# Kernel optimization log

Hardware: AMD Instinct MI355X
Metric: run time of the kernel (lower is better)

The kernel has to match this reference:

```python
import jax, jax.numpy as jnp
import numpy as np

N_NODES = 50000
N_EDGES = 800000
IN_DIM = 512
HEADS = 4
HID = 64
OUT = 64
NEG_SLOPE = 0.2  # DGL GATConv default


def gat_layer(x, W, attn_l, attn_r, bias, src, dst, n_nodes, heads, d_out):
    # x: [N, F_in], W: [F_in, heads*d_out], attn_l/attn_r: [heads, d_out], bias: [heads, d_out]
    f = (x @ W).reshape(n_nodes, heads, d_out)          # [N, H, D]
    el = jnp.sum(f * attn_l, axis=-1)                   # [N, H]
    er = jnp.sum(f * attn_r, axis=-1)                   # [N, H]
    e = jax.nn.leaky_relu(el[src] + er[dst], NEG_SLOPE) # [E, H]
    # segment softmax over incoming edges of each dst node
    m = jax.ops.segment_max(e, dst, num_segments=n_nodes)       # [N, H]
    ex = jnp.exp(e - m[dst])                                     # [E, H]
    den = jax.ops.segment_sum(ex, dst, num_segments=n_nodes)    # [N, H]
    a = ex / den[dst]                                            # [E, H]
    # scatter-aggregate weighted messages
    out = jax.ops.segment_sum(a[:, :, None] * f[src], dst, num_segments=n_nodes)  # [N, H, D]
    return out + bias, a


def setup_inputs() -> dict:
    key = jax.random.key(0)
    ks = jax.random.split(key, 12)
    features = jax.random.normal(ks[0], (N_NODES, IN_DIM), dtype=jnp.float32)
    src = jax.random.randint(ks[1], (N_EDGES,), 0, N_NODES, dtype=jnp.int32)
    dst = jax.random.randint(ks[2], (N_EDGES,), 0, N_NODES, dtype=jnp.int32)
    s1 = 1.0 / np.sqrt(IN_DIM)
    s2 = 1.0 / np.sqrt(HEADS * HID)
    W1 = jax.random.normal(ks[3], (IN_DIM, HEADS * HID), dtype=jnp.float32) * s1
    al1 = jax.random.normal(ks[4], (HEADS, HID), dtype=jnp.float32) * s1
    ar1 = jax.random.normal(ks[5], (HEADS, HID), dtype=jnp.float32) * s1
    b1 = jnp.zeros((HEADS, HID), dtype=jnp.float32)
    W2 = jax.random.normal(ks[6], (HEADS * HID, OUT), dtype=jnp.float32) * s2
    al2 = jax.random.normal(ks[7], (1, OUT), dtype=jnp.float32) * s2
    ar2 = jax.random.normal(ks[8], (1, OUT), dtype=jnp.float32) * s2
    b2 = jnp.zeros((1, OUT), dtype=jnp.float32)
    return {"features": features, "W1": W1, "al1": al1, "ar1": ar1, "b1": b1,
            "W2": W2, "al2": al2, "ar2": ar2, "b2": b2, "src": src, "dst": dst}


def reference(features, W1, al1, ar1, b1, W2, al2, ar2, b2, src, dst):
    h1, _ = gat_layer(features, W1, al1, ar1, b1, src, dst, N_NODES, HEADS, HID)
    h1 = jax.nn.elu(h1.reshape(N_NODES, HEADS * HID))   # flatten heads + ELU
    h2, _ = gat_layer(h1, W2, al2, ar2, b2, src, dst, N_NODES, 1, OUT)
    return h2  # [N, 1, OUT]
```

## Files before the change

### kernel.cpp

```cpp
#include <hip/hip_runtime.h>

#define N_NODES 50000
#define N_EDGES 800000
#define IN_DIM 512
#define NEG_SLOPE 0.2f

typedef short short8 __attribute__((ext_vector_type(8)));
typedef float f32x16 __attribute__((ext_vector_type(16)));
typedef __attribute__((address_space(3))) unsigned int lds_u32;
typedef const __attribute__((address_space(1))) unsigned int glb_u32;

__device__ __forceinline__ unsigned bf16rne(float f) {
  union { float f; unsigned u; } v;
  v.f = f;
  return (v.u + 0x7FFFu + ((v.u >> 16) & 1u)) >> 16;
}
__device__ __forceinline__ void tsplit8(float4 a, float4 b, short8& hi,
                                        short8& lo) {
  float fa[8] = {a.x, a.y, a.z, a.w, b.x, b.y, b.z, b.w};
#pragma unroll
  for (int i = 0; i < 8; i++) {
    unsigned u = __float_as_uint(fa[i]);
    hi[i] = (short)(u >> 16);
    float lof = fa[i] - __uint_as_float(u & 0xffff0000u);
    lo[i] = (short)(__float_as_uint(lof) >> 16);
  }
}

__global__ void pack_w(const float* __restrict__ W, short* __restrict__ Bhi,
                       int N) {
  int k = blockIdx.x, n = threadIdx.x;
  float w = W[(size_t)k * N + n];
  int ksub = k >> 4, kh = (k >> 3) & 1, j = k & 7;
  int nsub = n >> 5, lane2 = (n & 31) | (kh << 5);
  size_t off = (((size_t)ksub * (N >> 5) + nsub) * 64 + lane2) * 8 + j;
  Bhi[off] = (short)bf16rne(w);
}

template <int K, int NSUBS, int NTILES, int WAVES>
__global__ __launch_bounds__(WAVES * 64) void gemm_mfma(
    const float* __restrict__ A, const short* __restrict__ Bhi_,
    unsigned short* __restrict__ Cb, const float* __restrict__ alv,
    const float* __restrict__ arv, float2* __restrict__ elt,
    float2* __restrict__ ert, int M) {
  constexpr int N = NSUBS * 32;
  constexpr int RT = WAVES / NTILES;
  constexpr int BROWS = RT * 32;
  constexpr int T = K / 32;
  constexpr int MT = BROWS / (8 * WAVES);
  constexpr int GB = NSUBS * 2 / WAVES;
  constexpr int NSUBT = NSUBS / NTILES;
  constexpr int HPW = NSUBT / 2;
  constexpr int NHEADS = NSUBS / 2;
  constexpr int BSTEP_S = NSUBS * 1024;
  static_assert(MT * WAVES * 8 == BROWS, "A staging covers the tile");
  static_assert(GB * WAVES * 512 == BSTEP_S, "B staging covers the step");
  static_assert(MT + GB == 5 || MT + GB == 6, "vmcnt literal coverage");
  __shared__ float ldsA[2][BROWS * 32];
  __shared__ short ldsB[2][BSTEP_S];

  const int tid = threadIdx.x;
  const int lane = tid & 63;
  const int w = tid >> 6;
  const int l31 = lane & 31;
  const int half = lane >> 5;
  const int local_mt = w / NTILES;
  const int ntile = w % NTILES;
  const int block_row0 = blockIdx.x * BROWS;

  const float* gsrcA[MT];
#pragma unroll
  for (int q = 0; q < MT; q++) {
    int seg = w * MT + q;
    int r = seg * 8 + (lane >> 3);
    int c = (lane & 7) ^ (r & 7);
    int grow = block_row0 + r;
    if (grow > M - 1) grow = M - 1;
    gsrcA[q] = A + (size_t)grow * K + c * 4;
  }
  const short* bsrc = Bhi_ + lane * 8;

  const int arow = local_mt * 32 + l31;
  const int rs = arow & 7;

  f32x16 acc[NSUBT] = {};

  auto STAGE = [&](int b, int t) {
#pragma unroll
    for (int q = 0; q < MT; q++) {
      __builtin_amdgcn_global_load_lds((glb_u32*)(gsrcA[q] + t * 32),
                                       (lds_u32*)&ldsA[b][(w * MT + q) * 256],
                                       16, 0, 0);
    }
#pragma unroll
    for (int j = 0; j < GB; j++) {
      __builtin_amdgcn_global_load_lds(
          (glb_u32*)(bsrc + (size_t)t * BSTEP_S + (w * GB + j) * 512),
          (lds_u32*)&ldsB[b][(w * GB + j) * 512], 16, 0, 0);
    }
  };

  STAGE(0, 0);

  int buf = 0;
  for (int t = 0; t < T; t++) {
    if (t + 1 < T) {
      STAGE(buf ^ 1, t + 1);
      if constexpr (MT + GB == 5)
        asm volatile("s_waitcnt vmcnt(5)" ::: "memory");
      else
        asm volatile("s_waitcnt vmcnt(6)" ::: "memory");
    } else {
      asm volatile("s_waitcnt vmcnt(0)" ::: "memory");
    }
    __builtin_amdgcn_s_barrier();

    const float* lA = ldsA[buf];
    const short* lB = ldsB[buf];
    __builtin_amdgcn_s_setprio(1);
#pragma unroll
    for (int u = 0; u < 2; u++) {
      int c0 = u * 4 + half * 2;
      float4 a0 = *(const float4*)&lA[arow * 32 + (c0 ^ rs) * 4];
      float4 a1 = *(const float4*)&lA[arow * 32 + ((c0 + 1) ^ rs) * 4];
      short8 ah, al8;
      tsplit8(a0, a1, ah, al8);
#pragma unroll
      for (int j = 0; j < NSUBT; j++) {
        short8 cbj = *(const short8*)&lB[(u * NSUBS + ntile * NSUBT + j) * 512 +
                                         lane * 8];
        acc[j] = __builtin_amdgcn_mfma_f32_32x32x16_bf16(ah, cbj, acc[j], 0, 0, 0);
        acc[j] =
            __builtin_amdgcn_mfma_f32_32x32x16_bf16(al8, cbj, acc[j], 0, 0, 0);
      }
    }
    __builtin_amdgcn_s_setprio(0);
    asm volatile("s_waitcnt lgkmcnt(0)" ::: "memory");
    __builtin_amdgcn_s_barrier();
    buf ^= 1;
  }

  const int mrow0 = block_row0 + local_mt * 32;
#pragma unroll
  for (int h = 0; h < HPW; h++) {
    int c0 = ntile * NSUBT * 32 + 2 * h * 32 + l31;
    float wa0 = alv[c0], wa1 = alv[c0 + 32];
    float wr0 = arv[c0], wr1 = arv[c0 + 32];
#pragma unroll
    for (int r = 0; r < 16; r++) {
      int roff = (r & 3) + 8 * (r >> 2) + 4 * half;
      int row = mrow0 + roff;
      float v0 = acc[2 * h][r], v1 = acc[2 * h + 1][r];
      if (row < M) {
        Cb[(size_t)row * N + c0] = (unsigned short)bf16rne(v0);
        Cb[(size_t)row * N + c0 + 32] = (unsigned short)bf16rne(v1);
      }
      float elv = v0 * wa0 + v1 * wa1;
      float erv = v0 * wr0 + v1 * wr1;
#pragma unroll
      for (int off = 1; off < 32; off <<= 1) {
        elv += __shfl_xor(elv, off);
        erv += __shfl_xor(erv, off);
      }
      if (l31 == 0 && row < M) {
        int hg = ntile * HPW + h;
        elt[(size_t)row * NHEADS + hg] =
            make_float2(__expf(elv), __expf(NEG_SLOPE * elv));
        ert[(size_t)row * NHEADS + hg] =
            make_float2(__expf(erv), __expf(NEG_SLOPE * erv));
      }
    }
  }
}

__global__ void hist_kernel(const int* __restrict__ dst,
                            int* __restrict__ counts) {
  int e = blockIdx.x * blockDim.x + threadIdx.x;
  if (e < N_EDGES) atomicAdd(&counts[dst[e]], 1);
}

#define NSCAN 196
__global__ __launch_bounds__(256) void scan_part(const int* __restrict__ counts,
                                                 int* __restrict__ offsets,
                                                 int* __restrict__ bsums) {
  __shared__ int sh[256];
  int t = threadIdx.x;
  int i = blockIdx.x * 256 + t;
  int v = (i < N_NODES) ? counts[i] : 0;
  sh[t] = v;
  __syncthreads();
  for (int o = 1; o < 256; o <<= 1) {
    int x = (t >= o) ? sh[t - o] : 0;
    __syncthreads();
    sh[t] += x;
    __syncthreads();
  }
  if (i < N_NODES) offsets[i] = sh[t] - v;
  if (t == 255) bsums[blockIdx.x] = sh[255];
}
__global__ __launch_bounds__(256) void scan_top(int* __restrict__ bsums) {
  __shared__ int sh[256];
  int t = threadIdx.x;
  int v = (t < NSCAN) ? bsums[t] : 0;
  sh[t] = v;
  __syncthreads();
  for (int o = 1; o < 256; o <<= 1) {
    int x = (t >= o) ? sh[t - o] : 0;
    __syncthreads();
    sh[t] += x;
    __syncthreads();
  }
  if (t < NSCAN) bsums[t] = sh[t] - v;
}
__global__ __launch_bounds__(256) void scan_add(int* __restrict__ offsets,
                                                const int* __restrict__ bsums) {
  int i = blockIdx.x * 256 + threadIdx.x;
  if (i < N_NODES) offsets[i] += bsums[blockIdx.x];
  if (i == 0) offsets[N_NODES] = N_EDGES;
}

__global__ void scatter_kernel(const int* __restrict__ src,
                               const int* __restrict__ dst,
                               const int* __restrict__ offsets,
                               int* __restrict__ fill,
                               int* __restrict__ csr_src) {
  int e = blockIdx.x * blockDim.x + threadIdx.x;
  if (e < N_EDGES) {
    int d = dst[e];
    int pos = offsets[d] + atomicAdd(&fill[d], 1);
    csr_src[pos] = src[e];
  }
}

#define AGG1_PROC(P0, P1, P2, P3, Q0, Q1, Q2, Q3)                        \
  do {                                                                   \
    float t0 = Q0.x * fv.x, u0 = Q0.y * fv.y;                            \
    float t1 = Q1.x * fv.x, u1 = Q1.y * fv.y;                            \
    float t2 = Q2.x * fv.x, u2 = Q2.y * fv.y;                            \
    float t3 = Q3.x * fv.x, u3 = Q3.y * fv.y;                            \
    float a0 = t0 > 1.f ? t0 : u0;                                       \
    float a1 = t1 > 1.f ? t1 : u1;                                       \
    float a2 = t2 > 1.f ? t2 : u2;                                       \
    float a3 = t3 > 1.f ? t3 : u3;                                       \
    sden += a0 + a2;                                                     \
    sden2 += a1 + a3;                                                    \
    acc.x += a0 * __uint_as_float(P0.x << 16);                           \
    acc.y += a0 * __uint_as_float(P0.x & 0xffff0000u);                   \
    acc.z += a0 * __uint_as_float(P0.y << 16);                           \
    acc.w += a0 * __uint_as_float(P0.y & 0xffff0000u);                   \
    acc2.x += a1 * __uint_as_float(P1.x << 16);                          \
    acc2.y += a1 * __uint_as_float(P1.x & 0xffff0000u);                  \
    acc2.z += a1 * __uint_as_float(P1.y << 16);                          \
    acc2.w += a1 * __uint_as_float(P1.y & 0xffff0000u);                  \
    acc.x += a2 * __uint_as_float(P2.x << 16);                           \
    acc.y += a2 * __uint_as_float(P2.x & 0xffff0000u);                   \
    acc.z += a2 * __uint_as_float(P2.y << 16);                           \
    acc.w += a2 * __uint_as_float(P2.y & 0xffff0000u);                   \
    acc2.x += a3 * __uint_as_float(P3.x << 16);                          \
    acc2.y += a3 * __uint_as_float(P3.x & 0xffff0000u);                  \
    acc2.z += a3 * __uint_as_float(P3.y << 16);                          \
    acc2.w += a3 * __uint_as_float(P3.y & 0xffff0000u);                  \
  } while (0)

__global__ __launch_bounds__(256) void agg1_kernel(
    const int* __restrict__ offsets, const int* __restrict__ csr_src,
    const float2* __restrict__ elt, const float2* __restrict__ ert,
    const unsigned short* __restrict__ fb, const float* __restrict__ bias,
    float* __restrict__ h1) {
  int w = threadIdx.x >> 6, lane = threadIdx.x & 63;
  int n = blockIdx.x * 4 + w;
  if (n >= N_NODES) return;
  int h = lane >> 4;
  int off0 = offsets[n], deg = offsets[n + 1] - off0;
  float2 fv = ert[n * 4 + h];
  float4 acc = {0.f, 0.f, 0.f, 0.f};
  float4 acc2 = {0.f, 0.f, 0.f, 0.f};
  float sden = 0.f, sden2 = 0.f;
  const unsigned short* fbl = fb + lane * 4;

  int i = 0;
  uint2 cp0, cp1, cp2, cp3;
  float2 cq0, cq1, cq2, cq3;
  bool have = (3 < deg);
  if (have) {
    int s0 = csr_src[off0], s1 = csr_src[off0 + 1];
    int s2 = csr_src[off0 + 2], s3 = csr_src[off0 + 3];
    cp0 = *(const uint2*)(fbl + (size_t)s0 * 256);
    cp1 = *(const uint2*)(fbl + (size_t)s1 * 256);
    cp2 = *(const uint2*)(fbl + (size_t)s2 * 256);
    cp3 = *(const uint2*)(fbl + (size_t)s3 * 256);
    cq0 = elt[s0 * 4 + h];
    cq1 = elt[s1 * 4 + h];
    cq2 = elt[s2 * 4 + h];
    cq3 = elt[s3 * 4 + h];
    i = 4;
  }
  for (; i + 3 < deg; i += 4) {
    int s0 = csr_src[off0 + i], s1 = csr_src[off0 + i + 1];
    int s2 = csr_src[off0 + i + 2], s3 = csr_src[off0 + i + 3];
    uint2 np0 = *(const uint2*)(fbl + (size_t)s0 * 256);
    uint2 np1 = *(const uint2*)(fbl + (size_t)s1 * 256);
    uint2 np2 = *(const uint2*)(fbl + (size_t)s2 * 256);
    uint2 np3 = *(const uint2*)(fbl + (size_t)s3 * 256);
    float2 nq0 = elt[s0 * 4 + h];
    float2 nq1 = elt[s1 * 4 + h];
    float2 nq2 = elt[s2 * 4 + h];
    float2 nq3 = elt[s3 * 4 + h];
    AGG1_PROC(cp0, cp1, cp2, cp3, cq0, cq1, cq2, cq3);
    cp0 = np0; cp1 = np1; cp2 = np2; cp3 = np3;
    cq0 = nq0; cq1 = nq1; cq2 = nq2; cq3 = nq3;
  }
  if (have) {
    AGG1_PROC(cp0, cp1, cp2, cp3, cq0, cq1, cq2, cq3);
  }
  for (; i < deg; i++) {
    int s0 = csr_src[off0 + i];
    uint2 p0 = *(const uint2*)(fbl + (size_t)s0 * 256);
    float2 q0 = elt[s0 * 4 + h];
    float t0 = q0.x * fv.x, u0 = q0.y * fv.y;
    float a0 = t0 > 1.f ? t0 : u0;
    sden += a0;
    acc.x += a0 * __uint_as_float(p0.x << 16);
    acc.y += a0 * __uint_as_float(p0.x & 0xffff0000u);
    acc.z += a0 * __uint_as_float(p0.y << 16);
    acc.w += a0 * __uint_as_float(p0.y & 0xffff0000u);
  }
  acc.x += acc2.x;
  acc.y += acc2.y;
  acc.z += acc2.z;
  acc.w += acc2.w;
  sden += sden2;
  float invd = sden > 0.f ? 1.0f / sden : 0.f;
  float4 b = ((const float4*)bias)[lane];
  float o[4] = {acc.x * invd + b.x, acc.y * invd + b.y, acc.z * invd + b.z,
                acc.w * invd + b.w};
#pragma unroll
  for (int j = 0; j < 4; j++) o[j] = o[j] > 0.f ? o[j] : __expf(o[j]) - 1.0f;
  float4 ov = {o[0], o[1], o[2], o[3]};
  *(float4*)(h1 + (size_t)n * 256 + lane * 4) = ov;
}
#undef AGG1_PROC

__global__ __launch_bounds__(256) void agg2_kernel(
    const int* __restrict__ offsets, const int* __restrict__ csr_src,
    const float2* __restrict__ elt, const float2* __restrict__ ert,
    const unsigned short* __restrict__ fb2, const float* __restrict__ bias,
    float* __restrict__ out) {
  int w = threadIdx.x >> 6, lane = threadIdx.x & 63;
  int n = blockIdx.x * 4 + w;
  if (n >= N_NODES) return;
  int dg = lane & 15, eslot = lane >> 4;
  int off0 = offsets[n], deg = offsets[n + 1] - off0;
  float2 fv = ert[n];
  float4 acc = {0.f, 0.f, 0.f, 0.f};
  float4 acc2 = {0.f, 0.f, 0.f, 0.f};
  float sden = 0.f;
  int i = eslot;
  for (; i + 4 < deg; i += 8) {
    int s0 = csr_src[off0 + i];
    int s1 = csr_src[off0 + i + 4];
    uint2 p0 = *(const uint2*)(fb2 + (size_t)s0 * 64 + dg * 4);
    uint2 p1 = *(const uint2*)(fb2 + (size_t)s1 * 64 + dg * 4);
    float2 q0 = elt[s0];
    float2 q1 = elt[s1];
    float t10 = q0.x * fv.x, t20 = q0.y * fv.y;
    float t11 = q1.x * fv.x, t21 = q1.y * fv.y;
    float a0 = t10 > 1.f ? t10 : t20;
    float a1 = t11 > 1.f ? t11 : t21;
    sden += a0 + a1;
    acc.x += a0 * __uint_as_float(p0.x << 16);
    acc.y += a0 * __uint_as_float(p0.x & 0xffff0000u);
    acc.z += a0 * __uint_as_float(p0.y << 16);
    acc.w += a0 * __uint_as_float(p0.y & 0xffff0000u);
    acc2.x += a1 * __uint_as_float(p1.x << 16);
    acc2.y += a1 * __uint_as_float(p1.x & 0xffff0000u);
    acc2.z += a1 * __uint_as_float(p1.y << 16);
    acc2.w += a1 * __uint_as_float(p1.y & 0xffff0000u);
  }
  if (i < deg) {
    int s0 = csr_src[off0 + i];
    uint2 p0 = *(const uint2*)(fb2 + (size_t)s0 * 64 + dg * 4);
    float2 q0 = elt[s0];
    float t10 = q0.x * fv.x, t20 = q0.y * fv.y;
    float a0 = t10 > 1.f ? t10 : t20;
    sden += a0;
    acc.x += a0 * __uint_as_float(p0.x << 16);
    acc.y += a0 * __uint_as_float(p0.x & 0xffff0000u);
    acc.z += a0 * __uint_as_float(p0.y << 16);
    acc.w += a0 * __uint_as_float(p0.y & 0xffff0000u);
  }
  acc.x += acc2.x;
  acc.y += acc2.y;
  acc.z += acc2.z;
  acc.w += acc2.w;
#pragma unroll
  for (int off = 16; off < 64; off <<= 1) {
    acc.x += __shfl_xor(acc.x, off);
    acc.y += __shfl_xor(acc.y, off);
    acc.z += __shfl_xor(acc.z, off);
    acc.w += __shfl_xor(acc.w, off);
    sden += __shfl_xor(sden, off);
  }
  if (eslot == 0) {
    float invd = sden > 0.f ? 1.0f / sden : 0.f;
    float4 b = ((const float4*)bias)[dg];
    float4 ov = {acc.x * invd + b.x, acc.y * invd + b.y, acc.z * invd + b.z,
                 acc.w * invd + b.w};
    *(float4*)(out + (size_t)n * 64 + dg * 4) = ov;
  }
}

extern "C" void kernel_launch(void* const* d_in, const int* in_sizes, int n_in,
                              void* d_out, int out_size, void* d_ws,
                              size_t ws_size, hipStream_t stream) {
  const float* features = (const float*)d_in[0];
  const float* W1 = (const float*)d_in[1];
  const float* al1 = (const float*)d_in[2];
  const float* ar1 = (const float*)d_in[3];
  const float* b1 = (const float*)d_in[4];
  const float* W2 = (const float*)d_in[5];
  const float* al2 = (const float*)d_in[6];
  const float* ar2 = (const float*)d_in[7];
  const float* b2 = (const float*)d_in[8];
  const int* src = (const int*)d_in[9];
  const int* dst = (const int*)d_in[10];
  float* out = (float*)d_out;

  float* h1 = (float*)d_ws;
  unsigned short* fb = (unsigned short*)(h1 + (size_t)N_NODES * 256);
  unsigned short* fb2 = fb;
  float2* elt1 = (float2*)(fb + (size_t)N_NODES * 256);
  float2* ert1 = elt1 + (size_t)N_NODES * 4;
  float2* elt2 = ert1 + (size_t)N_NODES * 4;
  float2* ert2 = elt2 + N_NODES;
  int* counts = (int*)(ert2 + N_NODES);
  int* offsets = counts + N_NODES;
  int* fill = offsets + N_NODES + 1;
  int* csr_src = fill + N_NODES;
  int* bsums = csr_src + N_EDGES;

  short* b1hi = (short*)d_out;
  short* b2hi = (short*)fill;

  hipMemsetAsync(counts, 0, N_NODES * sizeof(int), stream);
  hipMemsetAsync(fill, 0, N_NODES * sizeof(int), stream);
  hist_kernel<<<(N_EDGES + 255) / 256, 256, 0, stream>>>(dst, counts);
  scan_part<<<NSCAN, 256, 0, stream>>>(counts, offsets, bsums);
  scan_top<<<1, 256, 0, stream>>>(bsums);
  scan_add<<<NSCAN, 256, 0, stream>>>(offsets, bsums);
  scatter_kernel<<<(N_EDGES + 255) / 256, 256, 0, stream>>>(src, dst, offsets,
                                                            fill, csr_src);

  pack_w<<<512, 256, 0, stream>>>(W1, b1hi, 256);
  pack_w<<<256, 64, 0, stream>>>(W2, b2hi, 64);

  gemm_mfma<IN_DIM, 8, 4, 4><<<1563, 256, 0, stream>>>(
      features, b1hi, fb, al1, ar1, elt1, ert1, N_NODES);
  agg1_kernel<<<(N_NODES + 3) / 4, 256, 0, stream>>>(offsets, csr_src, elt1,
                                                     ert1, fb, b1, h1);

  gemm_mfma<256, 2, 1, 2><<<782, 128, 0, stream>>>(h1, b2hi, fb2, al2, ar2,
                                                   elt2, ert2, N_NODES);
  agg2_kernel<<<(N_NODES + 3) / 4, 256, 0, stream>>>(offsets, csr_src, elt2,
                                                     ert2, fb2, b2, out);
}
```

Before: 410.3 us.

## Emit layer-1 output pre-split into MFMA fragment layout for register-only layer-2 GEMM

The first aggregation kernel now writes h1 as separate bf16 hi and lo planes, already in the MFMA A-operand fragment order. This replaces the fp32 store and the split that was done later. A new single-wave gemm2_reg kernel then loads these fragments and the packed W2 straight into registers, with no LDS staging or barriers, and computes the second projection along with the attention logits. It also drops the s_setprio hints in the first GEMM. The aim is to cut layer-2 GEMM traffic and sync overhead. The cost is tiny 64-thread blocks and uncoalesced-looking short4 stores in agg1.

```diff
diff --git a/kernel.cpp b/kernel.cpp
--- a/kernel.cpp
+++ b/kernel.cpp
@@ -4,6 +4,7 @@
 #define N_EDGES 800000
 #define IN_DIM 512
 #define NEG_SLOPE 0.2f
+#define G1 1563
 
 typedef short short8 __attribute__((ext_vector_type(8)));
 typedef float f32x16 __attribute__((ext_vector_type(16)));
@@ -117,7 +118,6 @@
 
     const float* lA = ldsA[buf];
     const short* lB = ldsB[buf];
-    __builtin_amdgcn_s_setprio(1);
 #pragma unroll
     for (int u = 0; u < 2; u++) {
       int c0 = u * 4 + half * 2;
@@ -134,7 +134,6 @@
             __builtin_amdgcn_mfma_f32_32x32x16_bf16(al8, cbj, acc[j], 0, 0, 0);
       }
     }
-    __builtin_amdgcn_s_setprio(0);
     asm volatile("s_waitcnt lgkmcnt(0)" ::: "memory");
     __builtin_amdgcn_s_barrier();
     buf ^= 1;
@@ -169,6 +168,56 @@
         ert[(size_t)row * NHEADS + hg] =
             make_float2(__expf(erv), __expf(NEG_SLOPE * erv));
       }
+    }
+  }
+}
+
+__global__ __launch_bounds__(64) void gemm2_reg(
+    const short* __restrict__ Ahi, const short* __restrict__ Alo,
+    const short* __restrict__ Bhi, unsigned short* __restrict__ Cb,
+    const float* __restrict__ alv, const float* __restrict__ arv,
+    float2* __restrict__ elt, float2* __restrict__ ert, int M) {
+  const int lane = threadIdx.x & 63;
+  const int g = blockIdx.x;
+  const int l31 = lane & 31;
+  const int half = lane >> 5;
+  const short8* ah = (const short8*)Ahi + (size_t)g * 16 * 64 + lane;
+  const short8* al = (const short8*)Alo + (size_t)g * 16 * 64 + lane;
+  const short8* bh = (const short8*)Bhi + lane;
+  f32x16 acc0 = {}, acc1 = {};
+#pragma unroll 4
+  for (int ks = 0; ks < 16; ks++) {
+    short8 a_hi = ah[ks * 64];
+    short8 a_lo = al[ks * 64];
+    short8 b0 = bh[(ks * 2) * 64];
+    short8 b1 = bh[(ks * 2 + 1) * 64];
+    acc0 = __builtin_amdgcn_mfma_f32_32x32x16_bf16(a_hi, b0, acc0, 0, 0, 0);
+    acc0 = __builtin_amdgcn_mfma_f32_32x32x16_bf16(a_lo, b0, acc0, 0, 0, 0);
+    acc1 = __builtin_amdgcn_mfma_f32_32x32x16_bf16(a_hi, b1, acc1, 0, 0, 0);
+    acc1 = __builtin_amdgcn_mfma_f32_32x32x16_bf16(a_lo, b1, acc1, 0, 0, 0);
+  }
+  float wa0 = alv[l31], wa1 = alv[l31 + 32];
+  float wr0 = arv[l31], wr1 = arv[l31 + 32];
+  const int mrow0 = g * 32;
+#pragma unroll
+  for (int r = 0; r < 16; r++) {
+    int roff = (r & 3) + 8 * (r >> 2) + 4 * half;
+    int row = mrow0 + roff;
+    float v0 = acc0[r], v1 = acc1[r];
+    if (row < M) {
+      Cb[(size_t)row * 64 + l31] = (unsigned short)bf16rne(v0);
+      Cb[(size_t)row * 64 + l31 + 32] = (unsigned short)bf16rne(v1);
+    }
+    float elv = v0 * wa0 + v1 * wa1;
+    float erv = v0 * wr0 + v1 * wr1;
+#pragma unroll
+    for (int off = 1; off < 32; off <<= 1) {
+      elv += __shfl_xor(elv, off);
+      erv += __shfl_xor(erv, off);
+    }
+    if (l31 == 0 && row < M) {
+      elt[row] = make_float2(__expf(elv), __expf(NEG_SLOPE * elv));
+      ert[row] = make_float2(__expf(erv), __expf(NEG_SLOPE * erv));
     }
   }
 }
@@ -266,7 +315,7 @@
     const int* __restrict__ offsets, const int* __restrict__ csr_src,
     const float2* __restrict__ elt, const float2* __restrict__ ert,
     const unsigned short* __restrict__ fb, const float* __restrict__ bias,
-    float* __restrict__ h1) {
+    short* __restrict__ h1hi, short* __restrict__ h1lo) {
   int w = threadIdx.x >> 6, lane = threadIdx.x & 63;
   int n = blockIdx.x * 4 + w;
   if (n >= N_NODES) return;
@@ -336,8 +385,19 @@
                 acc.w * invd + b.w};
 #pragma unroll
   for (int j = 0; j < 4; j++) o[j] = o[j] > 0.f ? o[j] : __expf(o[j]) - 1.0f;
-  float4 ov = {o[0], o[1], o[2], o[3]};
-  *(float4*)(h1 + (size_t)n * 256 + lane * 4) = ov;
+  size_t base = (((size_t)(n >> 5) * 16 + (lane >> 2)) * 64 +
+                 ((n & 31) | (((lane >> 1) & 1) << 5))) * 8 +
+                (lane & 1) * 4;
+  short hi4[4], lo4[4];
+#pragma unroll
+  for (int j = 0; j < 4; j++) {
+    unsigned u = __float_as_uint(o[j]);
+    hi4[j] = (short)(u >> 16);
+    float lof = o[j] - __uint_as_float(u & 0xffff0000u);
+    lo4[j] = (short)(__float_as_uint(lof) >> 16);
+  }
+  *(short4*)(h1hi + base) = make_short4(hi4[0], hi4[1], hi4[2], hi4[3]);
+  *(short4*)(h1lo + base) = make_short4(lo4[0], lo4[1], lo4[2], lo4[3]);
 }
 #undef AGG1_PROC
 
@@ -426,8 +486,10 @@
   const int* dst = (const int*)d_in[10];
   float* out = (float*)d_out;
 
-  float* h1 = (float*)d_ws;
-  unsigned short* fb = (unsigned short*)(h1 + (size_t)N_NODES * 256);
+  constexpr size_t PLANE = (size_t)G1 * 16 * 64 * 8;
+  short* h1hi = (short*)d_ws;
+  short* h1lo = h1hi + PLANE;
+  unsigned short* fb = (unsigned short*)(h1lo + PLANE);
   unsigned short* fb2 = fb;
   float2* elt1 = (float2*)(fb + (size_t)N_NODES * 256);
   float2* ert1 = elt1 + (size_t)N_NODES * 4;
@@ -457,10 +519,10 @@
   gemm_mfma<IN_DIM, 8, 4, 4><<<1563, 256, 0, stream>>>(
       features, b1hi, fb, al1, ar1, elt1, ert1, N_NODES);
   agg1_kernel<<<(N_NODES + 3) / 4, 256, 0, stream>>>(offsets, csr_src, elt1,
-                                                     ert1, fb, b1, h1);
-
-  gemm_mfma<256, 2, 1, 2><<<782, 128, 0, stream>>>(h1, b2hi, fb2, al2, ar2,
-                                                   elt2, ert2, N_NODES);
+                                                     ert1, fb, b1, h1hi, h1lo);
+
+  gemm2_reg<<<G1, 64, 0, stream>>>(h1hi, h1lo, b2hi, fb2, al2, ar2, elt2,
+                                   ert2, N_NODES);
   agg2_kernel<<<(N_NODES + 3) / 4, 256, 0, stream>>>(offsets, csr_src, elt2,
                                                      ert2, fb2, b2, out);
 }
```

New measurement: 425.8 us. 1.04x slower.
